# Kernel optimization log

Measured on AMD Instinct MI355X. Metric: run time of the kernel, lower is better.

Reference implementation:

```python
import jax, jax.numpy as jnp
import numpy as np

B, M, P, L, L_EVAL = 16, 32, 16, 1024, 2048


def setup_inputs() -> dict:
    key = jax.random.key(0)
    ks = jax.random.split(key, 6)
    # sorted event times per (B, P) path via cumsum of positive steps
    steps = jax.random.uniform(ks[0], (B, P, L), minval=0.01, maxval=0.1)
    event_times = jnp.cumsum(steps, axis=-1)  # [B, P, L], strictly increasing
    norm_constants = jax.random.uniform(ks[1], (B,), minval=0.5, maxval=1.5)
    # queries on the ORIGINAL (unnormalised) time axis, spanning the event range
    t_max = event_times[..., -1]  # [B, P]
    q_norm = jax.random.uniform(ks[2], (B, P, L_EVAL)) * (1.05 * t_max)[..., None]
    query_times = q_norm * norm_constants[:, None, None]
    mu = jax.random.uniform(ks[3], (B, M, P, L), minval=0.05, maxval=1.0)
    alpha = jax.random.uniform(ks[4], (B, M, P, L), minval=0.05, maxval=2.0)
    beta = jax.random.uniform(ks[5], (B, M, P, L), minval=0.1, maxval=3.0)
    return {
        "query_times": query_times,
        "event_times": event_times,
        "mu": mu,
        "alpha": alpha,
        "beta": beta,
        "norm_constants": norm_constants,
    }


def _batched_searchsorted(a, v):
    # a: [B, P, L] sorted along last dim, v: [B, P, Q] -> int32 [B, P, Q]
    f = lambda av, vv: jnp.searchsorted(av, vv, side="left")
    return jax.vmap(jax.vmap(f))(a, v)


def reference(query_times, event_times, mu, alpha, beta, norm_constants):
    Bq, Pq, Le = query_times.shape
    Mm = mu.shape[1]
    # normalized_times=False path: map queries onto the normalised axis
    q_norm = query_times / norm_constants[:, None, None]  # [B, P, Le]
    # index of the latest event strictly before each query time
    last_idx = _batched_searchsorted(event_times, q_norm) - 1  # [B, P, Le]
    idx = jnp.clip(last_idx, 0, None)
    gidx = jnp.broadcast_to(idx[:, None, :, :], (Bq, Mm, Pq, Le))
    mu_last = jnp.take_along_axis(mu, gidx, axis=3)
    alpha_last = jnp.take_along_axis(alpha, gidx, axis=3)
    beta_last = jnp.take_along_axis(beta, gidx, axis=3)
    t_last = jnp.take_along_axis(event_times, idx, axis=2)  # [B, P, Le]
    t_last = jnp.where(last_idx == -1, jnp.zeros_like(t_last), t_last)
    delta_t = (q_norm - t_last)[:, None, :, :]  # [B, 1, P, Le]
    intensity = mu_last + (alpha_last - mu_last) * jnp.exp(-beta_last * delta_t)
    # map intensity back to the original scale
    intensity = intensity / norm_constants[:, None, None, None]
    return intensity
```

## Files before the change

kernel.cpp:

```cpp
#include <hip/hip_runtime.h>


constexpr int B  = 16;
constexpr int M  = 32;
constexpr int P  = 16;
constexpr int L  = 1024;
constexpr int LE = 2048;

__global__ __launch_bounds__(1024)
void hawkes_kernel(const float* __restrict__ qt,
                   const float* __restrict__ ev,
                   const float* __restrict__ mu,
                   const float* __restrict__ al,
                   const float* __restrict__ be,
                   const float* __restrict__ nc,
                   float* __restrict__ out)
{
    __shared__ float s_ev[L];
    __shared__ float s_mu[2][L];
    __shared__ float s_al[2][L];
    __shared__ float s_be[2][L];

    const int bp = blockIdx.x;
    const int b  = bp >> 4;
    const int p  = bp & (P - 1);
    const int t  = threadIdx.x;

    const float norm     = nc[b];
    const float inv_norm = (float)(1.0 / (double)norm);

    s_ev[t] = ev[(size_t)bp * L + t];

    const size_t row0 = ((size_t)b * M * P + p) * L;
    const size_t mstr = (size_t)P * L;
    s_mu[0][t] = mu[row0 + t];
    s_al[0][t] = al[row0 + t];
    s_be[0][t] = be[row0 + t];

    __syncthreads();

    const float* qrow = qt + (size_t)bp * LE;
    int   idx[2];
    float dt[2];
#pragma unroll
    for (int k = 0; k < 2; ++k) {
        const float qn = __fmul_rn(qrow[t + k * 1024], inv_norm);
        int lo = 0, hi = L;
        while (lo < hi) {
            const int mid = (lo + hi) >> 1;
            if (s_ev[mid] < qn) lo = mid + 1; else hi = mid;
        }
        const int last = lo - 1;
        const int   i  = (last < 0) ? 0    : last;
        const float tl = (last < 0) ? 0.0f : s_ev[last];
        idx[k] = i;
        dt[k]  = qn - tl;
    }

    const size_t obase0 = ((size_t)b * M * P + p) * LE;

    for (int m = 0; m < M; ++m) {
        __syncthreads();
        const int cur = m & 1;
        if (m + 1 < M) {
            const size_t r  = row0 + (size_t)(m + 1) * mstr;
            const int   nxt = cur ^ 1;
            s_mu[nxt][t] = mu[r + t];
            s_al[nxt][t] = al[r + t];
            s_be[nxt][t] = be[r + t];
        }
        float* orow = out + obase0 + (size_t)m * (P * LE);
#pragma unroll
        for (int k = 0; k < 2; ++k) {
            const float m0 = s_mu[cur][idx[k]];
            const float a0 = s_al[cur][idx[k]];
            const float b0 = s_be[cur][idx[k]];
            const float v  = fmaf(a0 - m0, __expf(-b0 * dt[k]), m0) * inv_norm;
            orow[t + k * 1024] = v;
        }
    }
}

extern "C" void kernel_launch(void* const* d_in, const int* in_sizes, int n_in,
                              void* d_out, int out_size, void* d_ws, size_t ws_size,
                              hipStream_t stream) {
    const float* qt = (const float*)d_in[0];
    const float* ev = (const float*)d_in[1];
    const float* mu = (const float*)d_in[2];
    const float* al = (const float*)d_in[3];
    const float* be = (const float*)d_in[4];
    const float* nc = (const float*)d_in[5];
    float* out = (float*)d_out;

    hawkes_kernel<<<B * P, 1024, 0, stream>>>(qt, ev, mu, al, be, nc, out);
}
```

Baseline: 35.18 us.

## Split M across four blocks per (b,p) and vectorize staging loads

The grid grows from 256 to 1024 blocks by giving each block a quarter of the M rows, and blocks shrink to 512 threads that each handle four queries. Staging loads into shared memory now use float2 vector loads. The aim is to fill more CUs on the GPU and shorten the serial M loop per block. The cost is that each block repeats the binary search over the queries, so search work is four times larger in total. Output row stride mstr*2 equals P*LE, so indexing stays correct.

```diff
diff --git a/kernel.cpp b/kernel.cpp
--- a/kernel.cpp
+++ b/kernel.cpp
@@ -6,8 +6,12 @@
 constexpr int P  = 16;
 constexpr int L  = 1024;
 constexpr int LE = 2048;
+constexpr int NC = 4;
+constexpr int MC = M / NC;
+constexpr int T  = 512;
+constexpr int QT = LE / T;
 
-__global__ __launch_bounds__(1024)
+__global__ __launch_bounds__(T)
 void hawkes_kernel(const float* __restrict__ qt,
                    const float* __restrict__ ev,
                    const float* __restrict__ mu,
@@ -21,30 +25,42 @@
     __shared__ float s_al[2][L];
     __shared__ float s_be[2][L];
 
-    const int bp = blockIdx.x;
-    const int b  = bp >> 4;
-    const int p  = bp & (P - 1);
-    const int t  = threadIdx.x;
+    const int bid = blockIdx.x;
+    const int bp  = bid >> 2;
+    const int mc  = bid & (NC - 1);
+    const int b   = bp >> 4;
+    const int p   = bp & (P - 1);
+    const int t   = threadIdx.x;
 
-    const float norm     = nc[b];
+    const float norm = nc[b];
     const float inv_norm = (float)(1.0 / (double)norm);
 
-    s_ev[t] = ev[(size_t)bp * L + t];
+    {
+        const float2 e2 = *reinterpret_cast<const float2*>(ev + (size_t)bp * L + 2 * t);
+        s_ev[2 * t]     = e2.x;
+        s_ev[2 * t + 1] = e2.y;
+    }
 
-    const size_t row0 = ((size_t)b * M * P + p) * L;
+    const size_t row0 = (((size_t)b * M + mc * MC) * P + p) * L;
     const size_t mstr = (size_t)P * L;
-    s_mu[0][t] = mu[row0 + t];
-    s_al[0][t] = al[row0 + t];
-    s_be[0][t] = be[row0 + t];
+
+    {
+        const float2 m2 = *reinterpret_cast<const float2*>(mu + row0 + 2 * t);
+        const float2 a2 = *reinterpret_cast<const float2*>(al + row0 + 2 * t);
+        const float2 b2 = *reinterpret_cast<const float2*>(be + row0 + 2 * t);
+        s_mu[0][2 * t] = m2.x; s_mu[0][2 * t + 1] = m2.y;
+        s_al[0][2 * t] = a2.x; s_al[0][2 * t + 1] = a2.y;
+        s_be[0][2 * t] = b2.x; s_be[0][2 * t + 1] = b2.y;
+    }
 
     __syncthreads();
 
     const float* qrow = qt + (size_t)bp * LE;
-    int   idx[2];
-    float dt[2];
+    int   idx[QT];
+    float dt[QT];
 #pragma unroll
-    for (int k = 0; k < 2; ++k) {
-        const float qn = __fmul_rn(qrow[t + k * 1024], inv_norm);
+    for (int j = 0; j < QT; ++j) {
+        const float qn = __fmul_rn(qrow[t + j * T], inv_norm);
         int lo = 0, hi = L;
         while (lo < hi) {
             const int mid = (lo + hi) >> 1;
@@ -53,30 +69,33 @@
         const int last = lo - 1;
         const int   i  = (last < 0) ? 0    : last;
         const float tl = (last < 0) ? 0.0f : s_ev[last];
-        idx[k] = i;
-        dt[k]  = qn - tl;
+        idx[j] = i;
+        dt[j]  = __fmul_rn(qn, 1.0f) - tl;
     }
 
-    const size_t obase0 = ((size_t)b * M * P + p) * LE;
+    const size_t obase0 = (((size_t)b * M + mc * MC) * P + p) * LE;
 
-    for (int m = 0; m < M; ++m) {
+    for (int mi = 0; mi < MC; ++mi) {
         __syncthreads();
-        const int cur = m & 1;
-        if (m + 1 < M) {
-            const size_t r  = row0 + (size_t)(m + 1) * mstr;
+        const int cur = mi & 1;
+        if (mi + 1 < MC) {
+            const size_t r  = row0 + (size_t)(mi + 1) * mstr;
             const int   nxt = cur ^ 1;
-            s_mu[nxt][t] = mu[r + t];
-            s_al[nxt][t] = al[r + t];
-            s_be[nxt][t] = be[r + t];
+            const float2 m2 = *reinterpret_cast<const float2*>(mu + r + 2 * t);
+            const float2 a2 = *reinterpret_cast<const float2*>(al + r + 2 * t);
+            const float2 b2 = *reinterpret_cast<const float2*>(be + r + 2 * t);
+            s_mu[nxt][2 * t] = m2.x; s_mu[nxt][2 * t + 1] = m2.y;
+            s_al[nxt][2 * t] = a2.x; s_al[nxt][2 * t + 1] = a2.y;
+            s_be[nxt][2 * t] = b2.x; s_be[nxt][2 * t + 1] = b2.y;
         }
-        float* orow = out + obase0 + (size_t)m * (P * LE);
+        float* orow = out + obase0 + (size_t)mi * mstr * 2;
 #pragma unroll
-        for (int k = 0; k < 2; ++k) {
-            const float m0 = s_mu[cur][idx[k]];
-            const float a0 = s_al[cur][idx[k]];
-            const float b0 = s_be[cur][idx[k]];
-            const float v  = fmaf(a0 - m0, __expf(-b0 * dt[k]), m0) * inv_norm;
-            orow[t + k * 1024] = v;
+        for (int j = 0; j < QT; ++j) {
+            const float m0 = s_mu[cur][idx[j]];
+            const float a0 = s_al[cur][idx[j]];
+            const float b0 = s_be[cur][idx[j]];
+            const float v  = fmaf(a0 - m0, __expf(-b0 * dt[j]), m0) * inv_norm;
+            orow[t + j * T] = v;
         }
     }
 }
@@ -92,5 +111,5 @@
     const float* nc = (const float*)d_in[5];
     float* out = (float*)d_out;
 
-    hawkes_kernel<<<B * P, 1024, 0, stream>>>(qt, ev, mu, al, be, nc, out);
+    hawkes_kernel<<<B * P * NC, T, 0, stream>>>(qt, ev, mu, al, be, nc, out);
 }
```

New measurement: 48.22 us. 37.1% more time.

## Prefetch parameter rows into registers two steps ahead and vectorize query/output access

Applied to the files above, without the earlier changes.

Reworks the per-m loop so global loads of mu/alpha/beta for upcoming rows go into registers one full iteration ahead of their shared-memory store. This hides global load latency behind compute and the barrier. Each thread now handles two adjacent queries, loaded with a float2 read and written with float2 stores. The two binary searches are interleaved in lockstep for more ILP. The cost is higher register pressure and a more complex double-buffer schedule.

```diff
diff --git a/kernel.cpp b/kernel.cpp
--- a/kernel.cpp
+++ b/kernel.cpp
@@ -29,55 +29,86 @@
     const float norm     = nc[b];
     const float inv_norm = (float)(1.0 / (double)norm);
 
-    s_ev[t] = ev[(size_t)bp * L + t];
-
     const size_t row0 = ((size_t)b * M * P + p) * L;
     const size_t mstr = (size_t)P * L;
-    s_mu[0][t] = mu[row0 + t];
-    s_al[0][t] = al[row0 + t];
-    s_be[0][t] = be[row0 + t];
+
+    const float e_in = ev[(size_t)bp * L + t];
+    float rA_mu = mu[row0 + t],        rA_al = al[row0 + t],        rA_be = be[row0 + t];
+    float rB_mu = mu[row0 + mstr + t], rB_al = al[row0 + mstr + t], rB_be = be[row0 + mstr + t];
+
+    s_ev[t]    = e_in;
+    s_mu[0][t] = rA_mu;  s_al[0][t] = rA_al;  s_be[0][t] = rA_be;
 
     __syncthreads();
 
-    const float* qrow = qt + (size_t)bp * LE;
+    const float2 q2 = *reinterpret_cast<const float2*>(qt + (size_t)bp * LE + 2 * t);
     int   idx[2];
-    float dt[2];
+    float dtv[2];
+    {
+        float qn[2] = { __fmul_rn(q2.x, inv_norm), __fmul_rn(q2.y, inv_norm) };
+        int lo[2] = {0, 0}, hi[2] = {L, L};
 #pragma unroll
-    for (int k = 0; k < 2; ++k) {
-        const float qn = __fmul_rn(qrow[t + k * 1024], inv_norm);
-        int lo = 0, hi = L;
-        while (lo < hi) {
-            const int mid = (lo + hi) >> 1;
-            if (s_ev[mid] < qn) lo = mid + 1; else hi = mid;
+        for (int s = 0; s < 11; ++s) {
+#pragma unroll
+            for (int k = 0; k < 2; ++k) {
+                if (lo[k] < hi[k]) {
+                    const int mid = (lo[k] + hi[k]) >> 1;
+                    if (s_ev[mid] < qn[k]) lo[k] = mid + 1; else hi[k] = mid;
+                }
+            }
         }
-        const int last = lo - 1;
-        const int   i  = (last < 0) ? 0    : last;
-        const float tl = (last < 0) ? 0.0f : s_ev[last];
-        idx[k] = i;
-        dt[k]  = qn - tl;
+#pragma unroll
+        for (int k = 0; k < 2; ++k) {
+            const int last = lo[k] - 1;
+            idx[k] = (last < 0) ? 0    : last;
+            const float tl = (last < 0) ? 0.0f : s_ev[idx[k]];
+            dtv[k] = qn[k] - tl;
+        }
     }
 
-    const size_t obase0 = ((size_t)b * M * P + p) * LE;
+    float* const obase = out + ((size_t)b * M * P + p) * LE + 2 * t;
 
-    for (int m = 0; m < M; ++m) {
+#pragma unroll 1
+    for (int m = 0; m < M; m += 2) {
+        if (m + 2 < M) {
+            const size_t r = row0 + (size_t)(m + 2) * mstr;
+            rA_mu = mu[r + t];  rA_al = al[r + t];  rA_be = be[r + t];
+        }
+        {
+            float2 o;
+            {
+                const float m0 = s_mu[0][idx[0]], a0 = s_al[0][idx[0]], b0 = s_be[0][idx[0]];
+                o.x = fmaf(a0 - m0, __expf(-b0 * dtv[0]), m0) * inv_norm;
+            }
+            {
+                const float m1 = s_mu[0][idx[1]], a1 = s_al[0][idx[1]], b1 = s_be[0][idx[1]];
+                o.y = fmaf(a1 - m1, __expf(-b1 * dtv[1]), m1) * inv_norm;
+            }
+            *reinterpret_cast<float2*>(obase + (size_t)m * (P * LE)) = o;
+        }
+        s_mu[1][t] = rB_mu;  s_al[1][t] = rB_al;  s_be[1][t] = rB_be;
         __syncthreads();
-        const int cur = m & 1;
-        if (m + 1 < M) {
-            const size_t r  = row0 + (size_t)(m + 1) * mstr;
-            const int   nxt = cur ^ 1;
-            s_mu[nxt][t] = mu[r + t];
-            s_al[nxt][t] = al[r + t];
-            s_be[nxt][t] = be[r + t];
+
+        if (m + 3 < M) {
+            const size_t r = row0 + (size_t)(m + 3) * mstr;
+            rB_mu = mu[r + t];  rB_al = al[r + t];  rB_be = be[r + t];
         }
-        float* orow = out + obase0 + (size_t)m * (P * LE);
-#pragma unroll
-        for (int k = 0; k < 2; ++k) {
-            const float m0 = s_mu[cur][idx[k]];
-            const float a0 = s_al[cur][idx[k]];
-            const float b0 = s_be[cur][idx[k]];
-            const float v  = fmaf(a0 - m0, __expf(-b0 * dt[k]), m0) * inv_norm;
-            orow[t + k * 1024] = v;
+        {
+            float2 o;
+            {
+                const float m0 = s_mu[1][idx[0]], a0 = s_al[1][idx[0]], b0 = s_be[1][idx[0]];
+                o.x = fmaf(a0 - m0, __expf(-b0 * dtv[0]), m0) * inv_norm;
+            }
+            {
+                const float m1 = s_mu[1][idx[1]], a1 = s_al[1][idx[1]], b1 = s_be[1][idx[1]];
+                o.y = fmaf(a1 - m1, __expf(-b1 * dtv[1]), m1) * inv_norm;
+            }
+            *reinterpret_cast<float2*>(obase + (size_t)(m + 1) * (P * LE)) = o;
         }
+        if (m + 2 < M) {
+            s_mu[0][t] = rA_mu;  s_al[0][t] = rA_al;  s_be[0][t] = rA_be;
+        }
+        __syncthreads();
     }
 }
 
```

After: 33.19 us. 5.6% less time.
